# Performance work log

Measured on AMD Instinct MI355X. Metric: run time of the kernel, lower is better.

The kernel has to match this reference:

```python
import jax, jax.numpy as jnp
import numpy as np

V = 30000
Y = 30000
D = 768
B = 8
N = 512
PAD_ID = 0
POS_EXPONENT = 1
NEG_INF = 1e12
LN_EPS = 1e-5


def setup_inputs() -> dict:
    key = jax.random.key(0)
    k1, k2, k3, k4, k5 = jax.random.split(key, 5)
    M_s = jax.random.randint(k1, (B, N), 0, V, dtype=jnp.int64)
    E_v = jax.random.normal(k2, (V, D), dtype=jnp.float32) * 0.02
    E_y = jax.random.normal(k3, (Y, D), dtype=jnp.float32) * 0.02
    # padding_idx=0 -> zero rows
    E_v = E_v.at[PAD_ID].set(0.0)
    E_y = E_y.at[PAD_ID].set(0.0)
    W_A = jax.random.normal(k4, (D, D), dtype=jnp.float32) * (1.0 / np.sqrt(D))
    W_O = jax.random.normal(k5, (D, D), dtype=jnp.float32) * (1.0 / np.sqrt(D))
    gamma = jnp.ones((D,), dtype=jnp.float32)
    beta = jnp.zeros((D,), dtype=jnp.float32)
    return {"M_s": M_s, "E_v": E_v, "E_y": E_y, "W_A": W_A, "W_O": W_O,
            "gamma": gamma, "beta": beta}


def positional_rep(seq_len: int, exponent: int) -> jnp.ndarray:
    idx = jnp.arange(seq_len)
    rel = (idx[None, :] - idx[:, None]).astype(jnp.float32)  # [N, N], j - i
    sign = jnp.where(rel >= 0, 1.0, -1.0)
    return sign * jnp.abs(rel) ** exponent


def layer_norm(x, gamma, beta):
    mu = jnp.mean(x, axis=-1, keepdims=True)
    var = jnp.mean((x - mu) ** 2, axis=-1, keepdims=True)
    return (x - mu) * jax.lax.rsqrt(var + LN_EPS) * gamma + beta


def reference(M_s, E_v, E_y, W_A, W_O, gamma, beta):
    # Embedding lookup (dropout is identity at eval / p=0)
    X = E_v[M_s]                                   # [B, N, D]
    Q = X                                          # self-attention mode (v_q=None)
    mask = (M_s != PAD_ID)                         # [B, N]

    # attention: logits = (Q @ W_A) @ X^T + pos_bias, mask, softmax
    logits = jnp.einsum('bnd,bmd->bnm', Q @ W_A, X)  # [B, N, N]
    logits = logits + positional_rep(X.shape[1], POS_EXPONENT)[None]
    logits = jnp.where(mask[:, None, :], logits, -NEG_INF)
    A = jax.nn.softmax(logits, axis=-1)            # [B, N, N]
    Q_c = jnp.einsum('bnm,bmd->bnd', A, X @ W_O)   # [B, N, D]

    H = layer_norm(Q_c + Q, gamma, beta)           # [B, N, D]
    y_logits = jnp.einsum('bnd,yd->bny', H, E_y)   # [B, N, Y]
    return y_logits, A
```

## Files before the change

kernel.cpp:

```cpp
#include <hip/hip_runtime.h>
#include <hip/hip_bf16.h>

using bf16 = __hip_bfloat16;
typedef __attribute__((ext_vector_type(8))) short bf16x8;
typedef __attribute__((ext_vector_type(4))) float f32x4;

#define DEV __device__ __forceinline__

#define AS1 __attribute__((address_space(1)))
#define AS3 __attribute__((address_space(3)))
#define SB  __builtin_amdgcn_sched_barrier(0)
#define BARR __builtin_amdgcn_s_barrier()
#define LG0 asm volatile("s_waitcnt lgkmcnt(0)" ::: "memory")
#define VM3 asm volatile("s_waitcnt vmcnt(3)" ::: "memory")
#define VM1 asm volatile("s_waitcnt vmcnt(1)" ::: "memory")
#define VM0 asm volatile("s_waitcnt vmcnt(0)" ::: "memory")

static constexpr int Bsz = 8, Nseq = 512, Dm = 768, Vv = 30000, Yv = 30000;
static constexpr int Ypad = 30208;
static constexpr int Tok = Bsz * Nseq;
static constexpr int NT = Dm / 32;

__global__ __launch_bounds__(512, 4)
void gemm_big(const bf16* __restrict__ Ag, const bf16* __restrict__ Bg,
              float* __restrict__ Cg)
{
    __shared__ bf16 sm[6][4096];

    int bid = blockIdx.x;
    { int cpx = gridDim.x >> 3; bid = (bid & 7) * cpx + (bid >> 3); }
    const int mT = bid & 31;
    const int nT = bid >> 5;

    const int tid  = threadIdx.x;
    const int lane = tid & 63;
    const int wid  = tid >> 6;
    const int wm   = wid >> 2;
    const int wn   = wid & 3;

    const int lr = tid >> 2;
    const int sc = ((tid & 3) ^ (lr & 3)) << 3;
    const bf16* aS  = Ag + (long)(mT * 128 + lr) * Dm + sc;
    const bf16* bS0 = Bg + (long)(nT * 256 + lr) * Dm + sc;
    const bf16* bS1 = bS0 + (long)128 * Dm;
    const int ldsW = wid << 9;

    const int fl = lane & 15;
    const int fh = lane >> 4;
    const int e0 = (fh ^ (fl & 3)) << 3;
    const int aro = (wm * 64 + fl) * 32;
    const int bro = (wn * 32 + fl) * 32;

    bf16x8 afr[4], bfr[2];
    f32x4 acc[4][2][2] = {};

#define STG(CI, PTR, T)                                                        \
    __builtin_amdgcn_global_load_lds((const AS1 void*)((PTR) + (T) * 32),      \
        (AS3 void*)&sm[CI][ldsW], 16, 0, 0);
#define RA(CI)                                                                 \
    _Pragma("unroll") for (int mm = 0; mm < 4; ++mm)                           \
        afr[mm] = *(const bf16x8*)&sm[CI][aro + mm * 512 + e0];
#define RB(CI)                                                                 \
    _Pragma("unroll") for (int nn = 0; nn < 2; ++nn)                           \
        bfr[nn] = *(const bf16x8*)&sm[CI][bro + nn * 512 + e0];
#define MF8(NQ)                                                                \
    __builtin_amdgcn_s_setprio(1);                                             \
    _Pragma("unroll") for (int mm = 0; mm < 4; ++mm)                           \
    _Pragma("unroll") for (int nn = 0; nn < 2; ++nn)                           \
        acc[mm][NQ][nn] = __builtin_amdgcn_mfma_f32_16x16x32_bf16(             \
            afr[mm], bfr[nn], acc[mm][NQ][nn], 0, 0, 0);                       \
    __builtin_amdgcn_s_setprio(0);

    STG(0, aS, 0) STG(1, bS0, 0) STG(2, bS1, 0) STG(3, aS, 1) STG(4, bS0, 1)
    VM3; SB; BARR; SB;

#pragma unroll 1
    for (int t = 0; t < NT - 2; t += 2) {
        RA(0) RB(1)
        STG(5, bS1, t + 1)
        VM3; SB; BARR; LG0; SB;
        MF8(0)
        SB; BARR; SB;
        RB(2)
        STG(0, aS, t + 2) STG(1, bS0, t + 2)
        VM3; SB; BARR; LG0; SB;
        MF8(1)
        SB; BARR; SB;
        RA(3) RB(4)
        STG(2, bS1, t + 2)
        VM3; SB; BARR; LG0; SB;
        MF8(0)
        SB; BARR; SB;
        RB(5)
        STG(3, aS, t + 3) STG(4, bS0, t + 3)
        VM3; SB; BARR; LG0; SB;
        MF8(1)
        SB; BARR; SB;
    }

    {
        RA(0) RB(1)
        STG(5, bS1, NT - 1)
        VM3; SB; BARR; LG0; SB;
        MF8(0)
        SB; BARR; SB;
        RB(2)
        VM1; SB; BARR; LG0; SB;
        MF8(1)
        SB; BARR; SB;
        RA(3) RB(4)
        VM0; SB; BARR; LG0; SB;
        MF8(0)
        SB; BARR; SB;
        RB(5)
        SB; BARR; LG0; SB;
        MF8(1)
    }

    const int rB = mT * 128 + wm * 64 + fh * 4;
    const int cB = nT * 256 + wn * 32 + fl;
#pragma unroll
    for (int mm = 0; mm < 4; ++mm)
#pragma unroll
    for (int nq = 0; nq < 2; ++nq)
#pragma unroll
    for (int nn = 0; nn < 2; ++nn) {
        const int c = cB + nq * 128 + nn * 16;
        if (c >= Yv) continue;
        const int r = rB + mm * 16;
#pragma unroll
        for (int j = 0; j < 4; ++j)
            __builtin_nontemporal_store(acc[mm][nq][nn][j],
                                        Cg + (long)(r + j) * Yv + c);
    }
#undef STG
#undef RA
#undef RB
#undef MF8
}

template<bool STORE_BF16>
__global__ __launch_bounds__(256)
void gemm_bt(const bf16* __restrict__ Ag, const bf16* __restrict__ Bg,
             void* __restrict__ Cg, int M, int Nc, int K, int lda, int ldc,
             long sA, long sB, long sC)
{
    __shared__ bf16 As[128 * 32];
    __shared__ bf16 Bs[128 * 32];

    const int bz = blockIdx.z;
    const bf16* A  = Ag + (long)bz * sA;
    const bf16* Bm = Bg + (long)bz * sB;

    const int bid = blockIdx.x;
    const int nTilesM = M >> 7;
    const int mTile = bid % nTilesM;
    const int nTile = bid / nTilesM;

    const int tid  = threadIdx.x;
    const int wave = tid >> 6;
    const int lane = tid & 63;

    const int sRow = (wave << 4) + (lane >> 2);
    const int sCol = (lane & 3) << 3;

    const long aBase = (long)(mTile * 128) * lda;
    const long bBase = (long)(nTile * 128) * K;

    const int fl = lane & 15;
    const int fh = lane >> 4;
    const int wRow = (wave >> 1) << 6;
    const int wCol = (wave & 1) << 6;

    f32x4 acc[4][4] = {};

    for (int k0 = 0; k0 < K; k0 += 32) {
#pragma unroll
        for (int t = 0; t < 2; ++t) {
            const bf16* gA = A  + aBase + (long)(t * 64 + sRow) * lda + (k0 + sCol);
            const bf16* gB = Bm + bBase + (long)(t * 64 + sRow) * K + (k0 + sCol);
            bf16* lA = &As[(t * 64 + (wave << 4)) * 32];
            bf16* lB = &Bs[(t * 64 + (wave << 4)) * 32];
            __builtin_amdgcn_global_load_lds(
                (const AS1 void*)gA, (AS3 void*)lA, 16, 0, 0);
            __builtin_amdgcn_global_load_lds(
                (const AS1 void*)gB, (AS3 void*)lB, 16, 0, 0);
        }
        __syncthreads();

        bf16x8 af[4], bfg[4];
#pragma unroll
        for (int m = 0; m < 4; ++m)
            af[m] = *(const bf16x8*)&As[(wRow + m * 16 + fl) * 32 + fh * 8];
#pragma unroll
        for (int n = 0; n < 4; ++n)
            bfg[n] = *(const bf16x8*)&Bs[(wCol + n * 16 + fl) * 32 + fh * 8];
#pragma unroll
        for (int m = 0; m < 4; ++m)
#pragma unroll
            for (int n = 0; n < 4; ++n)
                acc[m][n] = __builtin_amdgcn_mfma_f32_16x16x32_bf16(
                    af[m], bfg[n], acc[m][n], 0, 0, 0);
        __syncthreads();
    }

    const int rBase = mTile * 128 + wRow + fh * 4;
    const int cBase = nTile * 128 + wCol + fl;
#pragma unroll
    for (int m = 0; m < 4; ++m) {
#pragma unroll
        for (int n = 0; n < 4; ++n) {
            int gc = cBase + n * 16;
            int gr = rBase + m * 16;
            if (STORE_BF16) {
                bf16* C = (bf16*)Cg + (long)bz * sC;
#pragma unroll
                for (int j = 0; j < 4; ++j)
                    C[(long)(gr + j) * ldc + gc] = __float2bfloat16(acc[m][n][j]);
            } else {
                float* C = (float*)Cg + (long)bz * sC;
#pragma unroll
                for (int j = 0; j < 4; ++j)
                    C[(long)(gr + j) * ldc + gc] = acc[m][n][j];
            }
        }
    }
}

__global__ __launch_bounds__(256) void k_cvt_ey(const float* __restrict__ Ey,
                                                bf16* __restrict__ Eyb)
{
    const long idx = ((long)blockIdx.x * 256 + threadIdx.x) * 8;
    const int row = (int)(idx / Dm);
    union { bf16 h[8]; uint4 u; } pk;
    if (row < Yv) {
        const f32x4* s = (const f32x4*)(Ey + idx);
        f32x4 a = __builtin_nontemporal_load(s);
        f32x4 b = __builtin_nontemporal_load(s + 1);
#pragma unroll
        for (int i = 0; i < 4; ++i) {
            pk.h[i]     = __float2bfloat16(a[i]);
            pk.h[4 + i] = __float2bfloat16(b[i]);
        }
    } else {
#pragma unroll
        for (int i = 0; i < 8; ++i) pk.h[i] = __float2bfloat16(0.f);
    }
    *(uint4*)(Eyb + idx) = pk.u;
}

__global__ void k_wT(const float* __restrict__ WA, const float* __restrict__ WO,
                     bf16* __restrict__ Wcat)
{
    __shared__ float t[32][33];
    const float* W = blockIdx.z ? WO : WA;
    bf16* WT = Wcat + (size_t)blockIdx.z * Dm * Dm;
    int bx = blockIdx.x * 32;
    int by = blockIdx.y * 32;
    int tx = threadIdx.x, ty = threadIdx.y;
#pragma unroll
    for (int i = 0; i < 32; i += 8)
        t[ty + i][tx] = W[(long)(bx + ty + i) * Dm + (by + tx)];
    __syncthreads();
#pragma unroll
    for (int i = 0; i < 32; i += 8)
        WT[(long)(by + ty + i) * Dm + (bx + tx)] = __float2bfloat16(t[tx][ty + i]);
}

__global__ __launch_bounds__(192) void k_gather(const int* __restrict__ Ms,
                                                const float* __restrict__ Ev,
                                                bf16* __restrict__ Xb)
{
    int token = blockIdx.x;
    int id = Ms[token];
    int d = threadIdx.x * 4;
    float4 v = *(const float4*)(Ev + (long)id * Dm + d);
    union { bf16 h[4]; uint2 u; } pk;
    pk.h[0] = __float2bfloat16(v.x); pk.h[1] = __float2bfloat16(v.y);
    pk.h[2] = __float2bfloat16(v.z); pk.h[3] = __float2bfloat16(v.w);
    *(uint2*)(Xb + (long)token * Dm + d) = pk.u;
}

__global__ void k_xwoT(const bf16* __restrict__ Xo, bf16* __restrict__ XoT)
{
    __shared__ bf16 t[32][33];
    int b = blockIdx.z;
    const bf16* src = Xo + (long)b * Nseq * 1536 + 768;
    bf16* dst = XoT + (long)b * Dm * Nseq;
    int bx = blockIdx.x * 32;
    int by = blockIdx.y * 32;
    int tx = threadIdx.x, ty = threadIdx.y;
#pragma unroll
    for (int i = 0; i < 32; i += 8)
        t[ty + i][tx] = src[(long)(bx + ty + i) * 1536 + (by + tx)];
    __syncthreads();
#pragma unroll
    for (int i = 0; i < 32; i += 8)
        dst[(long)(by + ty + i) * Nseq + (bx + tx)] = t[tx][ty + i];
}

DEV float waveMax(float v) {
#pragma unroll
    for (int o = 32; o > 0; o >>= 1) v = fmaxf(v, __shfl_xor(v, o, 64));
    return v;
}
DEV float waveSum(float v) {
#pragma unroll
    for (int o = 32; o > 0; o >>= 1) v += __shfl_xor(v, o, 64);
    return v;
}

__global__ __launch_bounds__(256) void k_softmax(const float* __restrict__ L,
                                                 const int* __restrict__ Ms,
                                                 float* __restrict__ Aout,
                                                 bf16* __restrict__ Ab)
{
    __shared__ float red[8];
    int row = blockIdx.x;
    int b = row >> 9, i = row & 511;
    const float* l = L + (long)row * Nseq;
    const int* ms = Ms + (b << 9);
    int t = threadIdx.x;
    int wid = t >> 6, lane = t & 63;
    int j0 = t, j1 = t + 256;

    float a0 = l[j0] + (float)(j0 - i);
    float a1 = l[j1] + (float)(j1 - i);
    if (ms[j0] == 0) a0 = -1e12f;
    if (ms[j1] == 0) a1 = -1e12f;

    float m = waveMax(fmaxf(a0, a1));
    if (lane == 0) red[wid] = m;
    __syncthreads();
    m = fmaxf(fmaxf(red[0], red[1]), fmaxf(red[2], red[3]));

    float e0 = expf(a0 - m), e1 = expf(a1 - m);
    float s = waveSum(e0 + e1);
    if (lane == 0) red[4 + wid] = s;
    __syncthreads();
    s = red[4] + red[5] + red[6] + red[7];
    float inv = 1.0f / s;

    float r0 = e0 * inv, r1 = e1 * inv;
    __builtin_nontemporal_store(r0, &Aout[(long)row * Nseq + j0]);
    __builtin_nontemporal_store(r1, &Aout[(long)row * Nseq + j1]);
    Ab[(long)row * Nseq + j0] = __float2bfloat16(r0);
    Ab[(long)row * Nseq + j1] = __float2bfloat16(r1);
}

__global__ __launch_bounds__(256) void k_ln(const float* __restrict__ Qc,
                                            const int* __restrict__ Ms,
                                            const float* __restrict__ Ev,
                                            const float* __restrict__ gamma,
                                            const float* __restrict__ beta,
                                            bf16* __restrict__ Hb)
{
    __shared__ float red[8];
    int row = blockIdx.x;
    int id = Ms[row];
    const float* q = Qc + (long)row * Dm;
    const float* e = Ev + (long)id * Dm;
    int t = threadIdx.x;
    int wid = t >> 6, lane = t & 63;

    float x[3];
#pragma unroll
    for (int c = 0; c < 3; ++c) x[c] = q[t + c * 256] + e[t + c * 256];

    float s = waveSum(x[0] + x[1] + x[2]);
    if (lane == 0) red[wid] = s;
    __syncthreads();
    float mu = (red[0] + red[1] + red[2] + red[3]) * (1.0f / 768.0f);

    float vs = 0.f;
#pragma unroll
    for (int c = 0; c < 3; ++c) { float d = x[c] - mu; vs += d * d; }
    vs = waveSum(vs);
    if (lane == 0) red[4 + wid] = vs;
    __syncthreads();
    float var = (red[4] + red[5] + red[6] + red[7]) * (1.0f / 768.0f);
    float rstd = rsqrtf(var + 1e-5f);

#pragma unroll
    for (int c = 0; c < 3; ++c) {
        int d = t + c * 256;
        Hb[(long)row * Dm + d] =
            __float2bfloat16((x[c] - mu) * rstd * gamma[d] + beta[d]);
    }
}

extern "C" void kernel_launch(void* const* d_in, const int* in_sizes, int n_in,
                              void* d_out, int out_size, void* d_ws, size_t ws_size,
                              hipStream_t stream)
{
    const int*   Ms    = (const int*)d_in[0];
    const float* Ev    = (const float*)d_in[1];
    const float* Ey    = (const float*)d_in[2];
    const float* WA    = (const float*)d_in[3];
    const float* WO    = (const float*)d_in[4];
    const float* gamma = (const float*)d_in[5];
    const float* beta  = (const float*)d_in[6];

    float* y_out = (float*)d_out;
    float* A_out = y_out + (size_t)Tok * Yv;

    char* ws = (char*)d_ws;
    size_t off = 0;
    auto alloc = [&](size_t n) { char* p = ws + off; off += (n + 255) & ~(size_t)255; return p; };
    bf16*  Xb    = (bf16*) alloc((size_t)Tok * Dm * 2);
    bf16*  WcatT = (bf16*) alloc((size_t)2 * Dm * Dm * 2);
    bf16*  QXWb  = (bf16*) alloc((size_t)Tok * 1536 * 2);
    bf16*  XWobT = (bf16*) alloc((size_t)Tok * Dm * 2);
    float* Lf    = (float*)alloc((size_t)Tok * Nseq * 4);
    bf16*  Ab    = (bf16*) alloc((size_t)Tok * Nseq * 2);
    float* Qc    = (float*)alloc((size_t)Tok * Dm * 4);
    bf16*  Hb    = (bf16*) alloc((size_t)Tok * Dm * 2);
    bf16*  Eyb   = (bf16*) alloc((size_t)Ypad * Dm * 2);

    k_cvt_ey<<<dim3(11328), dim3(256), 0, stream>>>(Ey, Eyb);
    k_wT<<<dim3(24, 24, 2), dim3(32, 8), 0, stream>>>(WA, WO, WcatT);
    k_gather<<<dim3(Tok), dim3(192), 0, stream>>>(Ms, Ev, Xb);
    gemm_bt<true><<<dim3(384), dim3(256), 0, stream>>>(
        Xb, WcatT, (void*)QXWb, Tok, 1536, Dm, Dm, 1536, 0L, 0L, 0L);
    gemm_bt<false><<<dim3(16, 1, 8), dim3(256), 0, stream>>>(
        QXWb, Xb, (void*)Lf, Nseq, Nseq, Dm, 1536, Nseq,
        (long)Nseq * 1536, (long)Nseq * Dm, (long)Nseq * Nseq);
    k_softmax<<<dim3(Tok), dim3(256), 0, stream>>>(Lf, Ms, A_out, Ab);
    k_xwoT<<<dim3(16, 24, 8), dim3(32, 8), 0, stream>>>(QXWb, XWobT);
    gemm_bt<false><<<dim3(24, 1, 8), dim3(256), 0, stream>>>(
        Ab, XWobT, (void*)Qc, Nseq, Dm, Nseq, Nseq, Dm,
        (long)Nseq * Nseq, (long)Dm * Nseq, (long)Nseq * Dm);
    k_ln<<<dim3(Tok), dim3(256), 0, stream>>>(Qc, Ms, Ev, gamma, beta, Hb);
    gemm_big<<<dim3(32 * (Ypad / 256)), dim3(512), 0, stream>>>(Hb, Eyb, y_out);
}
```

Measured before the change: 361.7 us.

## Merge prep kernels, add 64-row bf16 logits GEMM, read bf16 residual in LN

```diff
diff --git a/kernel.cpp b/kernel.cpp
--- a/kernel.cpp
+++ b/kernel.cpp
@@ -227,58 +227,137 @@
     }
 }
 
-__global__ __launch_bounds__(256) void k_cvt_ey(const float* __restrict__ Ey,
-                                                bf16* __restrict__ Eyb)
-{
-    const long idx = ((long)blockIdx.x * 256 + threadIdx.x) * 8;
-    const int row = (int)(idx / Dm);
-    union { bf16 h[8]; uint4 u; } pk;
-    if (row < Yv) {
-        const f32x4* s = (const f32x4*)(Ey + idx);
-        f32x4 a = __builtin_nontemporal_load(s);
-        f32x4 b = __builtin_nontemporal_load(s + 1);
-#pragma unroll
-        for (int i = 0; i < 4; ++i) {
-            pk.h[i]     = __float2bfloat16(a[i]);
-            pk.h[4 + i] = __float2bfloat16(b[i]);
+__global__ __launch_bounds__(256)
+void gemm_bt64(const bf16* __restrict__ Ag, const bf16* __restrict__ Bg,
+               bf16* __restrict__ Cg, int M, int K, int lda, int ldc,
+               long sA, long sB, long sC)
+{
+    __shared__ bf16 As[64 * 32];
+    __shared__ bf16 Bs[128 * 32];
+
+    const int bz = blockIdx.z;
+    const bf16* A  = Ag + (long)bz * sA;
+    const bf16* Bm = Bg + (long)bz * sB;
+    bf16* C = Cg + (long)bz * sC;
+
+    const int bid = blockIdx.x;
+    const int nTilesM = M >> 6;
+    const int mTile = bid % nTilesM;
+    const int nTile = bid / nTilesM;
+
+    const int tid  = threadIdx.x;
+    const int wave = tid >> 6;
+    const int lane = tid & 63;
+
+    const int sRow = tid >> 2;
+    const int sCol = (tid & 3) << 3;
+
+    const long aBase = (long)(mTile * 64) * lda;
+    const long bBase = (long)(nTile * 128) * K;
+
+    const int fl = lane & 15;
+    const int fh = lane >> 4;
+
+    f32x4 acc[4][2] = {};
+
+    for (int k0 = 0; k0 < K; k0 += 32) {
+        __builtin_amdgcn_global_load_lds(
+            (const AS1 void*)(A + aBase + (long)sRow * lda + (k0 + sCol)),
+            (AS3 void*)&As[wave * 512], 16, 0, 0);
+#pragma unroll
+        for (int t = 0; t < 2; ++t)
+            __builtin_amdgcn_global_load_lds(
+                (const AS1 void*)(Bm + bBase + (long)(t * 64 + sRow) * K + (k0 + sCol)),
+                (AS3 void*)&Bs[t * 2048 + wave * 512], 16, 0, 0);
+        __syncthreads();
+
+        bf16x8 af[4], bfg[2];
+#pragma unroll
+        for (int m = 0; m < 4; ++m)
+            af[m] = *(const bf16x8*)&As[(m * 16 + fl) * 32 + fh * 8];
+#pragma unroll
+        for (int n = 0; n < 2; ++n)
+            bfg[n] = *(const bf16x8*)&Bs[(wave * 32 + n * 16 + fl) * 32 + fh * 8];
+#pragma unroll
+        for (int m = 0; m < 4; ++m)
+#pragma unroll
+            for (int n = 0; n < 2; ++n)
+                acc[m][n] = __builtin_amdgcn_mfma_f32_16x16x32_bf16(
+                    af[m], bfg[n], acc[m][n], 0, 0, 0);
+        __syncthreads();
+    }
+
+    const int rBase = mTile * 64 + fh * 4;
+    const int cBase = nTile * 128 + wave * 32 + fl;
+#pragma unroll
+    for (int m = 0; m < 4; ++m)
+#pragma unroll
+    for (int n = 0; n < 2; ++n) {
+        const int gc = cBase + n * 16;
+        const int gr = rBase + m * 16;
+#pragma unroll
+        for (int j = 0; j < 4; ++j)
+            C[(long)(gr + j) * ldc + gc] = __float2bfloat16(acc[m][n][j]);
+    }
+}
+
+static constexpr int PREP_CVT = 11328, PREP_WT = 1152, PREP_GATHER = 4096;
+
+__global__ __launch_bounds__(256)
+void k_prep(const float* __restrict__ Ey, bf16* __restrict__ Eyb,
+            const float* __restrict__ WA, const float* __restrict__ WO,
+            bf16* __restrict__ Wcat,
+            const int* __restrict__ Ms, const float* __restrict__ Ev,
+            bf16* __restrict__ Xb)
+{
+    __shared__ float t[32][33];
+    const int b = blockIdx.x;
+    const int tid = threadIdx.x;
+
+    if (b < PREP_CVT) {
+        const long idx = ((long)b * 256 + tid) * 8;
+        const int row = (int)(idx / Dm);
+        union { bf16 h[8]; uint4 u; } pk;
+        if (row < Yv) {
+            const f32x4* s = (const f32x4*)(Ey + idx);
+            f32x4 a = __builtin_nontemporal_load(s);
+            f32x4 c = __builtin_nontemporal_load(s + 1);
+#pragma unroll
+            for (int i = 0; i < 4; ++i) {
+                pk.h[i]     = __float2bfloat16(a[i]);
+                pk.h[4 + i] = __float2bfloat16(c[i]);
+            }
+        } else {
+#pragma unroll
+            for (int i = 0; i < 8; ++i) pk.h[i] = __float2bfloat16(0.f);
         }
+        *(uint4*)(Eyb + idx) = pk.u;
+    } else if (b < PREP_CVT + PREP_WT) {
+        const int rem = b - PREP_CVT;
+        const int z = rem / 576, r2 = rem % 576;
+        const int bx = (r2 % 24) * 32, by = (r2 / 24) * 32;
+        const float* W = z ? WO : WA;
+        bf16* WT = Wcat + (size_t)z * Dm * Dm;
+        const int tx = tid & 31, ty = tid >> 5;
+#pragma unroll
+        for (int i = 0; i < 32; i += 8)
+            t[ty + i][tx] = W[(long)(bx + ty + i) * Dm + (by + tx)];
+        __syncthreads();
+#pragma unroll
+        for (int i = 0; i < 32; i += 8)
+            WT[(long)(by + ty + i) * Dm + (bx + tx)] = __float2bfloat16(t[tx][ty + i]);
     } else {
-#pragma unroll
-        for (int i = 0; i < 8; ++i) pk.h[i] = __float2bfloat16(0.f);
-    }
-    *(uint4*)(Eyb + idx) = pk.u;
-}
-
-__global__ void k_wT(const float* __restrict__ WA, const float* __restrict__ WO,
-                     bf16* __restrict__ Wcat)
-{
-    __shared__ float t[32][33];
-    const float* W = blockIdx.z ? WO : WA;
-    bf16* WT = Wcat + (size_t)blockIdx.z * Dm * Dm;
-    int bx = blockIdx.x * 32;
-    int by = blockIdx.y * 32;
-    int tx = threadIdx.x, ty = threadIdx.y;
-#pragma unroll
-    for (int i = 0; i < 32; i += 8)
-        t[ty + i][tx] = W[(long)(bx + ty + i) * Dm + (by + tx)];
-    __syncthreads();
-#pragma unroll
-    for (int i = 0; i < 32; i += 8)
-        WT[(long)(by + ty + i) * Dm + (bx + tx)] = __float2bfloat16(t[tx][ty + i]);
-}
-
-__global__ __launch_bounds__(192) void k_gather(const int* __restrict__ Ms,
-                                                const float* __restrict__ Ev,
-                                                bf16* __restrict__ Xb)
-{
-    int token = blockIdx.x;
-    int id = Ms[token];
-    int d = threadIdx.x * 4;
-    float4 v = *(const float4*)(Ev + (long)id * Dm + d);
-    union { bf16 h[4]; uint2 u; } pk;
-    pk.h[0] = __float2bfloat16(v.x); pk.h[1] = __float2bfloat16(v.y);
-    pk.h[2] = __float2bfloat16(v.z); pk.h[3] = __float2bfloat16(v.w);
-    *(uint2*)(Xb + (long)token * Dm + d) = pk.u;
+        const int token = b - (PREP_CVT + PREP_WT);
+        if (tid < 192) {
+            const int id = Ms[token];
+            const int d = tid * 4;
+            float4 v = *(const float4*)(Ev + (long)id * Dm + d);
+            union { bf16 h[4]; uint2 u; } pk;
+            pk.h[0] = __float2bfloat16(v.x); pk.h[1] = __float2bfloat16(v.y);
+            pk.h[2] = __float2bfloat16(v.z); pk.h[3] = __float2bfloat16(v.w);
+            *(uint2*)(Xb + (long)token * Dm + d) = pk.u;
+        }
+    }
 }
 
 __global__ void k_xwoT(const bf16* __restrict__ Xo, bf16* __restrict__ XoT)
@@ -310,7 +389,7 @@
     return v;
 }
 
-__global__ __launch_bounds__(256) void k_softmax(const float* __restrict__ L,
+__global__ __launch_bounds__(256) void k_softmax(const bf16* __restrict__ L,
                                                  const int* __restrict__ Ms,
                                                  float* __restrict__ Aout,
                                                  bf16* __restrict__ Ab)
@@ -318,14 +397,14 @@
     __shared__ float red[8];
     int row = blockIdx.x;
     int b = row >> 9, i = row & 511;
-    const float* l = L + (long)row * Nseq;
+    const bf16* l = L + (long)row * Nseq;
     const int* ms = Ms + (b << 9);
     int t = threadIdx.x;
     int wid = t >> 6, lane = t & 63;
     int j0 = t, j1 = t + 256;
 
-    float a0 = l[j0] + (float)(j0 - i);
-    float a1 = l[j1] + (float)(j1 - i);
+    float a0 = __bfloat162float(l[j0]) + (float)(j0 - i);
+    float a1 = __bfloat162float(l[j1]) + (float)(j1 - i);
     if (ms[j0] == 0) a0 = -1e12f;
     if (ms[j1] == 0) a1 = -1e12f;
 
@@ -349,23 +428,22 @@
 }
 
 __global__ __launch_bounds__(256) void k_ln(const float* __restrict__ Qc,
-                                            const int* __restrict__ Ms,
-                                            const float* __restrict__ Ev,
+                                            const bf16* __restrict__ Xb,
                                             const float* __restrict__ gamma,
                                             const float* __restrict__ beta,
                                             bf16* __restrict__ Hb)
 {
     __shared__ float red[8];
     int row = blockIdx.x;
-    int id = Ms[row];
     const float* q = Qc + (long)row * Dm;
-    const float* e = Ev + (long)id * Dm;
+    const bf16* e = Xb + (long)row * Dm;
     int t = threadIdx.x;
     int wid = t >> 6, lane = t & 63;
 
     float x[3];
 #pragma unroll
-    for (int c = 0; c < 3; ++c) x[c] = q[t + c * 256] + e[t + c * 256];
+    for (int c = 0; c < 3; ++c)
+        x[c] = q[t + c * 256] + __bfloat162float(e[t + c * 256]);
 
     float s = waveSum(x[0] + x[1] + x[2]);
     if (lane == 0) red[wid] = s;
@@ -411,25 +489,24 @@
     bf16*  WcatT = (bf16*) alloc((size_t)2 * Dm * Dm * 2);
     bf16*  QXWb  = (bf16*) alloc((size_t)Tok * 1536 * 2);
     bf16*  XWobT = (bf16*) alloc((size_t)Tok * Dm * 2);
-    float* Lf    = (float*)alloc((size_t)Tok * Nseq * 4);
+    bf16*  Lb    = (bf16*) alloc((size_t)Tok * Nseq * 2);
     bf16*  Ab    = (bf16*) alloc((size_t)Tok * Nseq * 2);
     float* Qc    = (float*)alloc((size_t)Tok * Dm * 4);
     bf16*  Hb    = (bf16*) alloc((size_t)Tok * Dm * 2);
     bf16*  Eyb   = (bf16*) alloc((size_t)Ypad * Dm * 2);
 
-    k_cvt_ey<<<dim3(11328), dim3(256), 0, stream>>>(Ey, Eyb);
-    k_wT<<<dim3(24, 24, 2), dim3(32, 8), 0, stream>>>(WA, WO, WcatT);
-    k_gather<<<dim3(Tok), dim3(192), 0, stream>>>(Ms, Ev, Xb);
+    k_prep<<<dim3(PREP_CVT + PREP_WT + PREP_GATHER), dim3(256), 0, stream>>>(
+        Ey, Eyb, WA, WO, WcatT, Ms, Ev, Xb);
     gemm_bt<true><<<dim3(384), dim3(256), 0, stream>>>(
         Xb, WcatT, (void*)QXWb, Tok, 1536, Dm, Dm, 1536, 0L, 0L, 0L);
-    gemm_bt<false><<<dim3(16, 1, 8), dim3(256), 0, stream>>>(
-        QXWb, Xb, (void*)Lf, Nseq, Nseq, Dm, 1536, Nseq,
+    gemm_bt64<<<dim3(32, 1, 8), dim3(256), 0, stream>>>(
+        QXWb, Xb, Lb, Nseq, Dm, 1536, Nseq,
         (long)Nseq * 1536, (long)Nseq * Dm, (long)Nseq * Nseq);
-    k_softmax<<<dim3(Tok), dim3(256), 0, stream>>>(Lf, Ms, A_out, Ab);
+    k_softmax<<<dim3(Tok), dim3(256), 0, stream>>>(Lb, Ms, A_out, Ab);
     k_xwoT<<<dim3(16, 24, 8), dim3(32, 8), 0, stream>>>(QXWb, XWobT);
     gemm_bt<false><<<dim3(24, 1, 8), dim3(256), 0, stream>>>(
         Ab, XWobT, (void*)Qc, Nseq, Dm, Nseq, Nseq, Dm,
         (long)Nseq * Nseq, (long)Dm * Nseq, (long)Nseq * Dm);
-    k_ln<<<dim3(Tok), dim3(256), 0, stream>>>(Qc, Ms, Ev, gamma, beta, Hb);
+    k_ln<<<dim3(Tok), dim3(256), 0, stream>>>(Qc, Xb, gamma, beta, Hb);
     gemm_big<<<dim3(32 * (Ypad / 256)), dim3(512), 0, stream>>>(Hb, Eyb, y_out);
 }
```

Result: faster. 350.1 us (-3.2%).
